# Kernel optimization log

Measured on AMD Instinct MI355X. Metric: run time of the kernel, lower is better.

Reference implementation:

```python
import jax, jax.numpy as jnp
import numpy as np

B, N, NODE_DIM, EDGE_DIM, H, L, Z, OUT = 4, 512, 16, 8, 64, 3, 64, 1
EPS = 1e-5  # torch BatchNorm1d default eps, training-mode batch stats


def _bn(x, g, b):
    # BatchNorm1d in training mode: biased batch mean/var over batch axis
    m = jnp.mean(x, axis=0)
    v = jnp.var(x, axis=0)
    return g * (x - m) * jax.lax.rsqrt(v + EPS) + b


def setup_inputs():
    keys = jax.random.split(jax.random.key(0), 16)

    def g(k, shape):
        fan = (shape[-2] + shape[-1]) if len(shape) >= 2 else 2 * shape[-1]
        return (jax.random.normal(k, shape) * np.sqrt(2.0 / fan)).astype(jnp.float32)

    return {
        'adj': (jax.random.uniform(keys[0], (B, N, N)) < 0.1).astype(jnp.float32),
        'node_feat': jax.random.normal(keys[1], (B, N, NODE_DIM), dtype=jnp.float32),
        'edge_feat': jax.random.normal(keys[2], (B, N, N, EDGE_DIM), dtype=jnp.float32),
        'nf1_w': g(keys[3], (NODE_DIM, 256)), 'nf1_b': jnp.zeros((256,), jnp.float32),
        'nf2_w': g(keys[4], (256, H)), 'nf2_b': jnp.zeros((H,), jnp.float32),
        'ef1_w': g(keys[5], (EDGE_DIM, 256)), 'ef1_b': jnp.zeros((256,), jnp.float32),
        'ef2_w': g(keys[6], (256, H)), 'ef2_b': jnp.zeros((H,), jnp.float32),
        'gcn_w': g(keys[7], (L, H, H)),
        'vn1_w': g(keys[8], (L, H, 2 * H)), 'vn1_b': jnp.zeros((L, 2 * H), jnp.float32),
        'vn1_g': jnp.ones((L, 2 * H), jnp.float32), 'vn1_be': jnp.zeros((L, 2 * H), jnp.float32),
        'vn2_w': g(keys[9], (L, 2 * H, H)), 'vn2_b': jnp.zeros((L, H), jnp.float32),
        'vn2_g': jnp.ones((L, H), jnp.float32), 'vn2_be': jnp.zeros((L, H), jnp.float32),
        'comb_w': g(keys[10], (L, 2 * H, H)), 'comb_b': jnp.zeros((L, H), jnp.float32),
        'lat1_w': g(keys[11], ((L + 1) * H, 256)), 'lat1_b': jnp.zeros((256,), jnp.float32),
        'lat2_w': g(keys[12], (256, Z)), 'lat2_b': jnp.zeros((Z,), jnp.float32),
        'fc1_w': g(keys[13], (Z, 512)), 'fc1_b': jnp.zeros((512,), jnp.float32),
        'fc2_w': g(keys[14], (512, OUT)), 'fc2_b': jnp.zeros((OUT,), jnp.float32),
    }


def _forward(adj, node_feat, edge_feat, nf1_w, nf1_b, nf2_w, nf2_b, ef1_w, ef1_b,
             ef2_w, ef2_b, gcn_w, vn1_w, vn1_b, vn1_g, vn1_be, vn2_w, vn2_b, vn2_g,
             vn2_be, comb_w, comb_b, lat1_w, lat1_b, lat2_w, lat2_b, fc1_w, fc1_b,
             fc2_w, fc2_b):
    # node / edge embedding MLPs
    nh = jnp.tanh(node_feat @ nf1_w + nf1_b)
    nh = jnp.tanh(nh @ nf2_w + nf2_b)                       # [B,N,H]
    eh = jnp.tanh(edge_feat @ ef1_w + ef1_b)
    eh = jnp.tanh(eh @ ef2_w + ef2_b)                       # [B,N,N,H]
    # einsum 'bijc,bjk->bik' sums over both j and c -> reduce c first
    e_sum = jnp.sum(eh, axis=-1)                            # [B,N,N]
    # GCN normalization: D = 1/rowsum(adj + I); identical every layer
    dinv = 1.0 / (jnp.sum(adj, axis=-1) + 1.0)
    adj_n = dinv[:, :, None] * adj                          # [B,N,N]
    hidden = nh
    alls = [nh]
    for l in range(L):
        hidden = jnp.tanh(adj_n @ (hidden @ gcn_w[l]))      # GraphConvSparse
        vn = jnp.mean(hidden, axis=1)                       # virtual-node pool [B,H]
        vn = jax.nn.relu(_bn(vn @ vn1_w[l] + vn1_b[l], vn1_g[l], vn1_be[l]))
        vn = jax.nn.relu(_bn(vn @ vn2_w[l] + vn2_b[l], vn2_g[l], vn2_be[l]))
        hidden = hidden + vn[:, None, :]                    # broadcast back to nodes
        gated = jnp.tanh(jnp.einsum('bij,bjk->bik', e_sum, hidden))
        hidden = jnp.tanh(jnp.concatenate([hidden, gated], axis=-1) @ comb_w[l] + comb_b[l])
        alls.append(hidden)
    lat = jnp.tanh(jnp.concatenate(alls, axis=-1) @ lat1_w + lat1_b)
    lat = jnp.tanh(lat @ lat2_w + lat2_b)                   # [B,N,Z]
    lat_sum = jnp.sum(lat, axis=1)                          # [B,Z]
    h = jnp.tanh(lat_sum @ fc1_w + fc1_b)
    predict = h @ fc2_w + fc2_b                             # [B,OUT]
    return predict, lat_sum


def reference(adj, node_feat, edge_feat, nf1_w, nf1_b, nf2_w, nf2_b, ef1_w, ef1_b,
              ef2_w, ef2_b, gcn_w, vn1_w, vn1_b, vn1_g, vn1_be, vn2_w, vn2_b, vn2_g,
              vn2_be, comb_w, comb_b, lat1_w, lat1_b, lat2_w, lat2_b, fc1_w, fc1_b,
              fc2_w, fc2_b):
    return _forward(adj, node_feat, edge_feat, nf1_w, nf1_b, nf2_w, nf2_b, ef1_w,
                    ef1_b, ef2_w, ef2_b, gcn_w, vn1_w, vn1_b, vn1_g, vn1_be, vn2_w,
                    vn2_b, vn2_g, vn2_be, comb_w, comb_b, lat1_w, lat1_b, lat2_w,
                    lat2_b, fc1_w, fc1_b, fc2_w, fc2_b)
```

## Files before the change

kernel.cpp:

```cpp
#include <hip/hip_runtime.h>
#include <math.h>

typedef unsigned short u16;
typedef unsigned int u32;

typedef __attribute__((ext_vector_type(8))) short short8;
typedef __attribute__((ext_vector_type(4))) float floatx4;

#define NTILES 16384

__device__ __forceinline__ float bfu(u16 u) { return __uint_as_float(((u32)u) << 16); }
__device__ __forceinline__ u16 f2bfs(float f) {
  u32 x = __float_as_uint(f);
  return (u16)((x + 0x7FFFu + ((x >> 16) & 1u)) >> 16);
}
__device__ __forceinline__ float tanh_fast(float x) {
  float e = __builtin_amdgcn_exp2f(x * 2.885390081777927f);
  return 1.0f - 2.0f * __builtin_amdgcn_rcpf(e + 1.0f);
}

__global__ __attribute__((amdgpu_flat_work_group_size(1024, 1024)))
__attribute__((amdgpu_waves_per_eu(4, 4)))
void k_edge(const float* __restrict__ ef,
    const float* __restrict__ w1, const float* __restrict__ b1,
    const float* __restrict__ w2, const float* __restrict__ b2,
    float* __restrict__ es32, u16* __restrict__ es16, int use16,
    int qt0, int qt1) {
  __shared__ __align__(16) short T1[16 * 2048];
  __shared__ __align__(16) short W2L[16384];
  __shared__ __align__(16) short W1L[2 * 2056];
  __shared__ __align__(16) float B1L[256];
  __shared__ __align__(16) float B2L[64];
  int t = threadIdx.x;
  int lane = t & 63, w = t >> 6, q = lane >> 4, r = lane & 15;

  for (int u = 0; u < 16; ++u) {
    int flat = u * 1024 + t;
    int k = flat >> 6, n = flat & 63;
    int c = k >> 3, j = k & 7;
    int physc = (c & 16) | ((c & 15) ^ (n & 15));
    W2L[(n * 32 + physc) * 8 + j] = (short)f2bfs(w2[flat]);
  }
  if (t < 512) {
    int hilo = t >> 8, idx = t & 255;
    int gu = idx >> 4, rr = idx & 15;
    int feat = (gu < 8) ? (rr * 8 + gu) : (120 + rr * 8 + gu);
    short8 v;
#pragma unroll
    for (int j = 0; j < 8; ++j) {
      float x = w1[j * 256 + feat];
      u32 xb = __float_as_uint(x);
      u16 hi = (u16)(xb >> 16);
      v[j] = hilo ? (short)f2bfs(x - bfu(hi)) : (short)hi;
    }
    *(short8*)&W1L[hilo * 2056 + idx * 8] = v;
  }
  if (t < 256) B1L[t] = b1[t];
  if (t < 64)  B2L[t] = b2[t];
  __syncthreads();

  short* t1w = &T1[w * 2048];
  const int hb = (q >> 1) * 2056;
  const int nw = gridDim.x * 16;
  int qt = qt0 + blockIdx.x * 16 + w;
  float4 e0, e1;
  {
    const float4* ep = (const float4*)(ef + (size_t)qt * 128 + (size_t)r * 8);
    e0 = ep[0]; e1 = ep[1];
  }

  for (; qt < qt1; qt += nw) {
    float ev[8] = {e0.x, e0.y, e0.z, e0.w, e1.x, e1.y, e1.z, e1.w};
    short8 af1;
#pragma unroll
    for (int j = 0; j < 8; ++j) {
      u32 xb = __float_as_uint(ev[j]);
      u16 hi = (u16)(xb >> 16);
      af1[j] = (q & 1) ? (short)f2bfs(ev[j] - bfu(hi)) : (short)hi;
    }
    int nqt = qt + nw;
    if (nqt < qt1) {
      const float4* ep = (const float4*)(ef + (size_t)nqt * 128 + (size_t)r * 8);
      e0 = ep[0]; e1 = ep[1];
    }
    floatx4 acc4[4];
#pragma unroll
    for (int nt = 0; nt < 4; ++nt) acc4[nt] = (floatx4){0.f, 0.f, 0.f, 0.f};
#pragma unroll
    for (int ph = 0; ph < 2; ++ph) {
      floatx4 c1[8];
#pragma unroll
      for (int u = 0; u < 8; ++u) c1[u] = (floatx4){0.f, 0.f, 0.f, 0.f};
#pragma unroll
      for (int u = 0; u < 8; ++u) {
        short8 bf = *(const short8*)&W1L[hb + ((ph * 8 + u) * 16 + r) * 8];
        c1[u] = __builtin_amdgcn_mfma_f32_16x16x32_bf16(af1, bf, c1[u], 0, 0, 0);
      }
      asm volatile("s_waitcnt lgkmcnt(0)" ::: "memory");
      __builtin_amdgcn_sched_barrier(0);
      const float4* bp = (const float4*)&B1L[ph * 128 + r * 8];
      float4 bA = bp[0], bB = bp[1];
      float bias[8] = {bA.x, bA.y, bA.z, bA.w, bB.x, bB.y, bB.z, bB.w};
#pragma unroll
      for (int reg = 0; reg < 4; ++reg) {
        u32 pk[4];
#pragma unroll
        for (int p2 = 0; p2 < 4; ++p2) {
          float va = tanh_fast(c1[2 * p2][reg] + bias[2 * p2]);
          float vb = tanh_fast(c1[2 * p2 + 1][reg] + bias[2 * p2 + 1]);
          u32 pr;
          asm("v_cvt_pk_bf16_f32 %0, %1, %2" : "=v"(pr) : "v"(va), "v"(vb));
          pk[p2] = pr;
        }
        int row = q * 4 + reg;
        int physc = r ^ row;
        int4 wa; wa.x = (int)pk[0]; wa.y = (int)pk[1]; wa.z = (int)pk[2]; wa.w = (int)pk[3];
        *(int4*)&t1w[(row * 16 + physc) * 8] = wa;
      }
      asm volatile("s_waitcnt lgkmcnt(0)" ::: "memory");
      __builtin_amdgcn_sched_barrier(0);
#pragma unroll
      for (int sm = 0; sm < 4; ++sm) {
        int cc = (4 * sm + q) ^ r;
        short8 af = *(const short8*)&t1w[(r * 16 + cc) * 8];
        int wc = ph * 16 + cc;
#pragma unroll
        for (int nt = 0; nt < 4; ++nt) {
          short8 bf = *(const short8*)&W2L[((nt * 16 + r) * 32 + wc) * 8];
          acc4[nt] = __builtin_amdgcn_mfma_f32_16x16x32_bf16(af, bf, acc4[nt], 0, 0, 0);
        }
      }
    }
    float s0 = 0.f, s1 = 0.f, s2 = 0.f, s3 = 0.f;
#pragma unroll
    for (int nt = 0; nt < 4; ++nt) {
      float bb = B2L[nt * 16 + r];
      s0 += tanh_fast(acc4[nt][0] + bb);
      s1 += tanh_fast(acc4[nt][1] + bb);
      s2 += tanh_fast(acc4[nt][2] + bb);
      s3 += tanh_fast(acc4[nt][3] + bb);
    }
#pragma unroll
    for (int off = 1; off < 16; off <<= 1) {
      s0 += __shfl_xor(s0, off, 64);
      s1 += __shfl_xor(s1, off, 64);
      s2 += __shfl_xor(s2, off, 64);
      s3 += __shfl_xor(s3, off, 64);
    }
    if (r == 0) {
      int base = qt * 16 + q * 4;
      if (use16) {
        es16[base] = f2bfs(s0); es16[base + 1] = f2bfs(s1);
        es16[base + 2] = f2bfs(s2); es16[base + 3] = f2bfs(s3);
      } else {
        float4 o; o.x = s0; o.y = s1; o.z = s2; o.w = s3;
        *(float4*)&es32[base] = o;
      }
    }
  }
}

__global__ __launch_bounds__(256) void k_pre(const float* __restrict__ nf,
    const float* __restrict__ w1, const float* __restrict__ b1,
    const float* __restrict__ w2, const float* __restrict__ b2,
    const float* __restrict__ gw, const float* __restrict__ adj,
    float* __restrict__ hid, u16* __restrict__ alls16, float* __restrict__ tmp,
    float* __restrict__ dinv, int* __restrict__ cnt) {
  __shared__ float nfx[4][16];
  __shared__ float t1[4][256];
  __shared__ float nh[4][64];
  int t = threadIdx.x;
  int node0 = blockIdx.x * 4;
  if (blockIdx.x == 0 && t < 16) cnt[t] = 0;
  if (t < 64) nfx[t >> 4][t & 15] = nf[node0 * 16 + t];
  __syncthreads();
  float b1t = b1[t];
  float a0 = b1t, a1 = b1t, a2 = b1t, a3 = b1t;
#pragma unroll
  for (int c = 0; c < 16; ++c) {
    float wv = w1[c * 256 + t];
    a0 += nfx[0][c] * wv; a1 += nfx[1][c] * wv;
    a2 += nfx[2][c] * wv; a3 += nfx[3][c] * wv;
  }
  t1[0][t] = tanh_fast(a0); t1[1][t] = tanh_fast(a1);
  t1[2][t] = tanh_fast(a2); t1[3][t] = tanh_fast(a3);
  __syncthreads();
  int nl = t >> 6, h = t & 63;
  {
    float acc = b2[h];
    for (int c = 0; c < 256; c += 4) {
      float4 xv = *(const float4*)&t1[nl][c];
      acc += xv.x * w2[c * 64 + h] + xv.y * w2[(c + 1) * 64 + h]
           + xv.z * w2[(c + 2) * 64 + h] + xv.w * w2[(c + 3) * 64 + h];
    }
    float v = tanh_fast(acc);
    int node = node0 + nl;
    hid[node * 64 + h] = v;
    alls16[node * 256 + h] = f2bfs(v);
    nh[nl][h] = v;
  }
  __syncthreads();
  {
    float g = 0.f;
    for (int c = 0; c < 64; ++c) g += nh[nl][c] * gw[c * 64 + h];
    tmp[(node0 + nl) * 64 + h] = g;
  }
  {
    int lane = t & 63, row = node0 + (t >> 6);
    float s = 0.f;
#pragma unroll
    for (int u = 0; u < 8; ++u) s += adj[(size_t)row * 512 + u * 64 + lane];
#pragma unroll
    for (int off = 32; off > 0; off >>= 1) s += __shfl_xor(s, off, 64);
    if (lane == 0) dinv[row] = 1.0f / (s + 1.0f);
  }
}

__global__ __launch_bounds__(256) void k_adjmm0(const float* __restrict__ adj,
    const float* __restrict__ X, const float* __restrict__ dinv,
    float* __restrict__ out, float* __restrict__ vnpart, int* cnt,
    const float* __restrict__ vw1, const float* __restrict__ vb1,
    const float* __restrict__ vg1, const float* __restrict__ vbe1,
    const float* __restrict__ vw2, const float* __restrict__ vb2,
    const float* __restrict__ vg2, const float* __restrict__ vbe2,
    float* __restrict__ vnout, int l) {
  __shared__ float Xt[64 * 64];
  __shared__ float Al[8 * 65];
  __shared__ floatx4 red4[256];
  __shared__ int isLast;
  int t = threadIdx.x;
  int b = blockIdx.x >> 6, it = blockIdx.x & 63;
  int hq = t & 15, slot = t >> 4, row = slot & 7, half = slot >> 3;
  floatx4 acc = (floatx4){0.f, 0.f, 0.f, 0.f};
  for (int jt = 0; jt < 8; ++jt) {
    __syncthreads();
    for (int u = 0; u < 16; ++u) {
      int idx = u * 256 + t;
      int jl = idx >> 6, hh = idx & 63;
      Xt[idx] = X[(b * 512 + jt * 64 + jl) * 64 + hh];
    }
#pragma unroll
    for (int u = 0; u < 2; ++u) {
      int idx = u * 256 + t;
      int il = idx >> 6, jl = idx & 63;
      Al[il * 65 + jl] = adj[((size_t)(b * 512 + it * 8 + il)) * 512 + jt * 64 + jl];
    }
    __syncthreads();
    const float* xp = &Xt[(half * 32) * 64 + hq * 4];
    const float* ap = &Al[row * 65 + half * 32];
#pragma unroll
    for (int jl = 0; jl < 32; ++jl) {
      floatx4 xv = *(const floatx4*)(xp + jl * 64);
      float a = ap[jl];
      acc[0] += a * xv[0]; acc[1] += a * xv[1];
      acc[2] += a * xv[2]; acc[3] += a * xv[3];
    }
  }
  red4[t] = acc;
  __syncthreads();
  if (t < 128) {
    floatx4 s = red4[t], s2 = red4[t + 128];
    int gr = b * 512 + it * 8 + row;
    float d = dinv[gr];
    floatx4 o;
#pragma unroll
    for (int i = 0; i < 4; ++i) o[i] = tanh_fast((s[i] + s2[i]) * d);
    *(floatx4*)&out[gr * 64 + hq * 4] = o;
    red4[t] = o;
  }
  __syncthreads();
  if (t < 16) {
    floatx4 ssum = (floatx4){0.f, 0.f, 0.f, 0.f};
#pragma unroll
    for (int r2 = 0; r2 < 8; ++r2) {
      floatx4 v = red4[r2 * 16 + t];
      ssum[0] += v[0]; ssum[1] += v[1]; ssum[2] += v[2]; ssum[3] += v[3];
    }
    *(floatx4*)&vnpart[(b * 64 + it) * 64 + t * 4] = ssum;
  }
  __threadfence();
  __syncthreads();
  if (t == 0) isLast = (atomicAdd(cnt, 1) == 255);
  __syncthreads();
  if (isLast) {
    __threadfence();
    float* x0 = Xt; float* x1 = Xt + 256; float* y1 = Xt + 768; float* x2 = Xt + 1280;
    {
      int bb = t >> 6, h = t & 63;
      float s = 0.f;
      for (int c = 0; c < 64; ++c) s += vnpart[(bb * 64 + c) * 64 + h];
      x0[t] = s * (1.0f / 512.0f);
    }
    __syncthreads();
    for (int rep = 0; rep < 2; ++rep) {
      int idx = rep * 256 + t;
      int bb = idx >> 7, j = idx & 127;
      float a = vb1[l * 128 + j];
      for (int h = 0; h < 64; ++h) a += x0[bb * 64 + h] * vw1[l * 8192 + h * 128 + j];
      x1[idx] = a;
    }
    __syncthreads();
    if (t < 128) {
      int j = t;
      float a = x1[j], bq = x1[128 + j], c = x1[256 + j], d = x1[384 + j];
      float m = 0.25f * (a + bq + c + d);
      float da = a - m, db = bq - m, dc = c - m, dd = d - m;
      float var = 0.25f * (da * da + db * db + dc * dc + dd * dd);
      float sc = vg1[l * 128 + j] / sqrtf(var + 1e-5f);
      float be = vbe1[l * 128 + j];
      y1[j]       = fmaxf(sc * da + be, 0.f);
      y1[128 + j] = fmaxf(sc * db + be, 0.f);
      y1[256 + j] = fmaxf(sc * dc + be, 0.f);
      y1[384 + j] = fmaxf(sc * dd + be, 0.f);
    }
    __syncthreads();
    {
      int bb = t >> 6, k = t & 63;
      float a = vb2[l * 64 + k];
      for (int j = 0; j < 128; ++j) a += y1[bb * 128 + j] * vw2[l * 8192 + j * 64 + k];
      x2[t] = a;
    }
    __syncthreads();
    if (t < 64) {
      int k = t;
      float a = x2[k], bq = x2[64 + k], c = x2[128 + k], d = x2[192 + k];
      float m = 0.25f * (a + bq + c + d);
      float da = a - m, db = bq - m, dc = c - m, dd = d - m;
      float var = 0.25f * (da * da + db * db + dc * dc + dd * dd);
      float sc = vg2[l * 64 + k] / sqrtf(var + 1e-5f);
      float be = vbe2[l * 64 + k];
      vnout[k]       = fmaxf(sc * da + be, 0.f);
      vnout[64 + k]  = fmaxf(sc * db + be, 0.f);
      vnout[128 + k] = fmaxf(sc * dc + be, 0.f);
      vnout[192 + k] = fmaxf(sc * dd + be, 0.f);
    }
  }
}

__global__ __launch_bounds__(256) void k_gate_comb(
    const float* __restrict__ es32, const u16* __restrict__ es16, int use16,
    const float* __restrict__ hid, const float* __restrict__ vnin,
    const float* __restrict__ cw, const float* __restrict__ cb,
    const float* __restrict__ gw_next,
    u16* __restrict__ alls16, float* __restrict__ tmpout, int l, int do_gcn) {
  __shared__ float Xt[64 * 64];
  __shared__ float Al[8 * 65];
  __shared__ floatx4 red4[256];
  __shared__ float gatedL[8 * 64];
  __shared__ float catL[8 * 128];
  __shared__ float hnL[8 * 64];
  int t = threadIdx.x;
  int b = blockIdx.x >> 6, it = blockIdx.x & 63;
  int hq = t & 15, slot = t >> 4, row = slot & 7, half = slot >> 3;
  floatx4 acc = (floatx4){0.f, 0.f, 0.f, 0.f};
  for (int jt = 0; jt < 8; ++jt) {
    __syncthreads();
    for (int u = 0; u < 16; ++u) {
      int idx = u * 256 + t;
      int jl = idx >> 6, hh = idx & 63;
      Xt[idx] = hid[(b * 512 + jt * 64 + jl) * 64 + hh] + vnin[b * 64 + hh];
    }
#pragma unroll
    for (int u = 0; u < 2; ++u) {
      int idx = u * 256 + t;
      int il = idx >> 6, jl = idx & 63;
      size_t ai = ((size_t)(b * 512 + it * 8 + il)) * 512 + jt * 64 + jl;
      Al[il * 65 + jl] = use16 ? bfu(es16[ai]) : es32[ai];
    }
    __syncthreads();
    const float* xp = &Xt[(half * 32) * 64 + hq * 4];
    const float* ap = &Al[row * 65 + half * 32];
#pragma unroll
    for (int jl = 0; jl < 32; ++jl) {
      floatx4 xv = *(const floatx4*)(xp + jl * 64);
      float a = ap[jl];
      acc[0] += a * xv[0]; acc[1] += a * xv[1];
      acc[2] += a * xv[2]; acc[3] += a * xv[3];
    }
  }
  red4[t] = acc;
  __syncthreads();
  if (t < 128) {
    floatx4 s = red4[t], s2 = red4[t + 128];
    floatx4 o;
#pragma unroll
    for (int i = 0; i < 4; ++i) o[i] = tanh_fast(s[i] + s2[i]);
    *(floatx4*)&gatedL[row * 64 + hq * 4] = o;
  }
  __syncthreads();
#pragma unroll
  for (int u = 0; u < 4; ++u) {
    int idx = u * 256 + t;
    int nl = idx >> 7, c = idx & 127;
    int node = b * 512 + it * 8 + nl;
    catL[idx] = (c < 64) ? (hid[node * 64 + c] + vnin[b * 64 + c])
                         : gatedL[nl * 64 + (c - 64)];
  }
  __syncthreads();
  int nl = t >> 6, h = t & 63;
  float a0 = cb[l * 64 + h], a1 = a0;
  const float* wp = cw + l * 8192 + h;
  for (int c = 0; c < 128; ++c) {
    float wv = wp[c * 64];
    a0 += catL[nl * 128 + c] * wv;
    a1 += catL[(nl + 4) * 128 + c] * wv;
  }
  float v0 = tanh_fast(a0), v1 = tanh_fast(a1);
  int n0 = b * 512 + it * 8 + nl, n1 = n0 + 4;
  alls16[n0 * 256 + (l + 1) * 64 + h] = f2bfs(v0);
  alls16[n1 * 256 + (l + 1) * 64 + h] = f2bfs(v1);
  if (do_gcn) {
    hnL[nl * 64 + h] = v0;
    hnL[(nl + 4) * 64 + h] = v1;
    __syncthreads();
    float g0 = 0.f, g1 = 0.f;
    for (int c = 0; c < 64; ++c) {
      float wv = gw_next[c * 64 + h];
      g0 += hnL[nl * 64 + c] * wv;
      g1 += hnL[(nl + 4) * 64 + c] * wv;
    }
    tmpout[n0 * 64 + h] = g0;
    tmpout[n1 * 64 + h] = g1;
  }
}

__global__ __launch_bounds__(512) void k_lat(const u16* __restrict__ alls16,
    const float* __restrict__ w1, const float* __restrict__ bb1,
    const float* __restrict__ w2, const float* __restrict__ bb2,
    float* __restrict__ latpart) {
  __shared__ float x[8][256];
  __shared__ float t1[8][256];
  __shared__ float red[8][256];
  int t = threadIdx.x;
  int g = t >> 8, tt = t & 255;
  int b = blockIdx.x >> 6, chunk = blockIdx.x & 63;
#pragma unroll
  for (int u = 0; u < 4; ++u)
    x[g * 4 + u][tt] = bfu(alls16[(size_t)(b * 512 + chunk * 8 + g * 4 + u) * 256 + tt]);
  __syncthreads();
  float a1[4];
  float bb = bb1[tt];
#pragma unroll
  for (int u = 0; u < 4; ++u) a1[u] = bb;
  for (int c = 0; c < 256; ++c) {
    float wv = w1[c * 256 + tt];
#pragma unroll
    for (int u = 0; u < 4; ++u) a1[u] += x[g * 4 + u][c] * wv;
  }
#pragma unroll
  for (int u = 0; u < 4; ++u) t1[g * 4 + u][tt] = tanh_fast(a1[u]);
  __syncthreads();
  int quar = tt >> 6, k = tt & 63, c0 = quar * 64;
  float a2[4];
#pragma unroll
  for (int u = 0; u < 4; ++u) a2[u] = 0.f;
  for (int c = 0; c < 64; ++c) {
    float wv = w2[(c0 + c) * 64 + k];
#pragma unroll
    for (int u = 0; u < 4; ++u) a2[u] += t1[g * 4 + u][c0 + c] * wv;
  }
#pragma unroll
  for (int u = 0; u < 4; ++u) red[g * 4 + u][tt] = a2[u];
  __syncthreads();
  if (t < 64) {
    float acc2 = 0.f;
    float b2v = bb2[t];
#pragma unroll
    for (int u = 0; u < 8; ++u) {
      float s = red[u][t] + red[u][t + 64] + red[u][t + 128] + red[u][t + 192] + b2v;
      acc2 += tanh_fast(s);
    }
    latpart[(b * 64 + chunk) * 64 + t] = acc2;
  }
}

__global__ __launch_bounds__(512) void k_final(const float* __restrict__ latpart,
    const float* __restrict__ f1w, const float* __restrict__ f1b,
    const float* __restrict__ f2w, const float* __restrict__ f2b,
    float* __restrict__ outp) {
  __shared__ float lred[512];
  __shared__ float ls[64];
  __shared__ float wred[8];
  int b = blockIdx.x, t = threadIdx.x;
  int z = t & 63, cg = t >> 6;
  float s = 0.f;
  for (int c = cg * 8; c < cg * 8 + 8; ++c) s += latpart[(b * 64 + c) * 64 + z];
  lred[t] = s;
  __syncthreads();
  if (t < 64) {
    float ssum = 0.f;
    for (int gg = 0; gg < 8; ++gg) ssum += lred[gg * 64 + t];
    ls[t] = ssum;
    outp[4 + b * 64 + t] = ssum;
  }
  __syncthreads();
  float acc = f1b[t];
  for (int zz = 0; zz < 64; ++zz) acc += ls[zz] * f1w[zz * 512 + t];
  float h = tanh_fast(acc);
  float p = h * f2w[t];
#pragma unroll
  for (int off = 32; off > 0; off >>= 1) p += __shfl_xor(p, off, 64);
  if ((t & 63) == 0) wred[t >> 6] = p;
  __syncthreads();
  if (t == 0) {
    float a = 0.f;
    for (int wv = 0; wv < 8; ++wv) a += wred[wv];
    outp[b] = a + f2b[0];
  }
}

extern "C" void kernel_launch(void* const* d_in, const int* in_sizes, int n_in,
                              void* d_out, int out_size, void* d_ws, size_t ws_size,
                              hipStream_t stream) {
  const float* adj       = (const float*)d_in[0];
  const float* node_feat = (const float*)d_in[1];
  const float* edge_feat = (const float*)d_in[2];
  const float* nf1_w = (const float*)d_in[3];
  const float* nf1_b = (const float*)d_in[4];
  const float* nf2_w = (const float*)d_in[5];
  const float* nf2_b = (const float*)d_in[6];
  const float* ef1_w = (const float*)d_in[7];
  const float* ef1_b = (const float*)d_in[8];
  const float* ef2_w = (const float*)d_in[9];
  const float* ef2_b = (const float*)d_in[10];
  const float* gcn_w = (const float*)d_in[11];
  const float* vn1_w = (const float*)d_in[12];
  const float* vn1_b = (const float*)d_in[13];
  const float* vn1_g = (const float*)d_in[14];
  const float* vn1_be = (const float*)d_in[15];
  const float* vn2_w = (const float*)d_in[16];
  const float* vn2_b = (const float*)d_in[17];
  const float* vn2_g = (const float*)d_in[18];
  const float* vn2_be = (const float*)d_in[19];
  const float* comb_w = (const float*)d_in[20];
  const float* comb_b = (const float*)d_in[21];
  const float* lat1_w = (const float*)d_in[22];
  const float* lat1_b = (const float*)d_in[23];
  const float* lat2_w = (const float*)d_in[24];
  const float* lat2_b = (const float*)d_in[25];
  const float* fc1_w = (const float*)d_in[26];
  const float* fc1_b = (const float*)d_in[27];
  const float* fc2_w = (const float*)d_in[28];
  const float* fc2_b = (const float*)d_in[29];

  const int use16 = (ws_size < (size_t)12 * 1024 * 1024) ? 1 : 0;
  char* p = (char*)d_ws;
  float* es32 = (float*)p;
  u16*   es16 = (u16*)p;
  size_t es_bytes = use16 ? (size_t)1048576 * 2 : (size_t)1048576 * 4;
  u16*   alls16  = (u16*)(p + es_bytes);
  float* hid     = (float*)(alls16 + 524288);
  float* tmp     = hid + 131072;
  float* dinv    = tmp + 131072;
  float* vnpart  = dinv + 2048;
  float* vn      = vnpart + 16384;
  float* latpart = vn + 256;
  int*   cnt     = (int*)(latpart + 16384);

  k_pre<<<512, 256, 0, stream>>>(node_feat, nf1_w, nf1_b, nf2_w, nf2_b,
                                 gcn_w, adj, hid, alls16, tmp, dinv, cnt);
  for (int d = 0; d < 8; ++d)
    k_edge<<<256, 1024, 0, stream>>>(edge_feat, ef1_w, ef1_b, ef2_w, ef2_b,
                                     es32, es16, use16,
                                     d * 8192, (d + 1) * 8192);
  for (int l = 0; l < 3; ++l) {
    k_adjmm0<<<256, 256, 0, stream>>>(adj, tmp, dinv, hid, vnpart, cnt + l,
        vn1_w, vn1_b, vn1_g, vn1_be, vn2_w, vn2_b, vn2_g, vn2_be, vn, l);
    k_gate_comb<<<256, 256, 0, stream>>>(es32, es16, use16, hid, vn,
        comb_w, comb_b, gcn_w + (l + 1) * 4096, alls16, tmp, l, (l < 2) ? 1 : 0);
  }
  k_lat<<<256, 512, 0, stream>>>(alls16, lat1_w, lat1_b, lat2_w, lat2_b, latpart);
  k_final<<<4, 512, 0, stream>>>(latpart, fc1_w, fc1_b, fc2_w, fc2_b,
                                 (float*)d_out);
}
```

Measured before the change: 468.5 us.

## Restructure adjacency matmuls to one wave per row with direct global loads

Rewrites the adj@X and edge-sum@hidden kernels so each 64-lane wave computes one output row, streaming the adjacency row as vector loads and reading X columns straight from global/L2 instead of staging tiles in shared memory. This doubles the grid to 512 blocks and drops most block-wide barriers. The virtual-node add is folded algebraically as rowsum(e)*vn, so it is no longer added per tile. The risk is more redundant global traffic for X, which no longer gets reuse from shared memory, and the wave-local LDS sync relies on s_waitcnt instead of __syncthreads.

```diff
diff --git a/kernel.cpp b/kernel.cpp
--- a/kernel.cpp
+++ b/kernel.cpp
@@ -224,71 +224,45 @@
     const float* __restrict__ vw2, const float* __restrict__ vb2,
     const float* __restrict__ vg2, const float* __restrict__ vbe2,
     float* __restrict__ vnout, int l) {
-  __shared__ float Xt[64 * 64];
-  __shared__ float Al[8 * 65];
-  __shared__ floatx4 red4[256];
+  __shared__ float vnp[4][64];
+  __shared__ float buf[1536];
   __shared__ int isLast;
   int t = threadIdx.x;
-  int b = blockIdx.x >> 6, it = blockIdx.x & 63;
-  int hq = t & 15, slot = t >> 4, row = slot & 7, half = slot >> 3;
-  floatx4 acc = (floatx4){0.f, 0.f, 0.f, 0.f};
-  for (int jt = 0; jt < 8; ++jt) {
-    __syncthreads();
-    for (int u = 0; u < 16; ++u) {
-      int idx = u * 256 + t;
-      int jl = idx >> 6, hh = idx & 63;
-      Xt[idx] = X[(b * 512 + jt * 64 + jl) * 64 + hh];
-    }
-#pragma unroll
-    for (int u = 0; u < 2; ++u) {
-      int idx = u * 256 + t;
-      int il = idx >> 6, jl = idx & 63;
-      Al[il * 65 + jl] = adj[((size_t)(b * 512 + it * 8 + il)) * 512 + jt * 64 + jl];
-    }
-    __syncthreads();
-    const float* xp = &Xt[(half * 32) * 64 + hq * 4];
-    const float* ap = &Al[row * 65 + half * 32];
-#pragma unroll
-    for (int jl = 0; jl < 32; ++jl) {
-      floatx4 xv = *(const floatx4*)(xp + jl * 64);
-      float a = ap[jl];
-      acc[0] += a * xv[0]; acc[1] += a * xv[1];
-      acc[2] += a * xv[2]; acc[3] += a * xv[3];
-    }
-  }
-  red4[t] = acc;
-  __syncthreads();
-  if (t < 128) {
-    floatx4 s = red4[t], s2 = red4[t + 128];
-    int gr = b * 512 + it * 8 + row;
-    float d = dinv[gr];
-    floatx4 o;
-#pragma unroll
-    for (int i = 0; i < 4; ++i) o[i] = tanh_fast((s[i] + s2[i]) * d);
-    *(floatx4*)&out[gr * 64 + hq * 4] = o;
-    red4[t] = o;
-  }
-  __syncthreads();
-  if (t < 16) {
-    floatx4 ssum = (floatx4){0.f, 0.f, 0.f, 0.f};
-#pragma unroll
-    for (int r2 = 0; r2 < 8; ++r2) {
-      floatx4 v = red4[r2 * 16 + t];
-      ssum[0] += v[0]; ssum[1] += v[1]; ssum[2] += v[2]; ssum[3] += v[3];
-    }
-    *(floatx4*)&vnpart[(b * 64 + it) * 64 + t * 4] = ssum;
+  int w = t >> 6, lane = t & 63;
+  int b = blockIdx.x >> 7, blk = blockIdx.x & 127;
+  int row = b * 512 + blk * 4 + w;
+  float d = dinv[row];
+  const float* ar = adj + (size_t)row * 512;
+  const float* xb = X + (size_t)b * 512 * 64;
+  float acc = 0.f;
+#pragma unroll 4
+  for (int j = 0; j < 512; j += 4) {
+    float4 a4 = *(const float4*)(ar + j);
+    float x0 = xb[(j + 0) * 64 + lane];
+    float x1 = xb[(j + 1) * 64 + lane];
+    float x2 = xb[(j + 2) * 64 + lane];
+    float x3 = xb[(j + 3) * 64 + lane];
+    acc += a4.x * x0 + a4.y * x1 + a4.z * x2 + a4.w * x3;
+  }
+  float o = tanh_fast(acc * d);
+  out[(size_t)row * 64 + lane] = o;
+  vnp[w][lane] = o;
+  __syncthreads();
+  if (t < 64) {
+    float s = vnp[0][t] + vnp[1][t] + vnp[2][t] + vnp[3][t];
+    vnpart[(b * 128 + blk) * 64 + t] = s;
   }
   __threadfence();
   __syncthreads();
-  if (t == 0) isLast = (atomicAdd(cnt, 1) == 255);
+  if (t == 0) isLast = (atomicAdd(cnt, 1) == 511);
   __syncthreads();
   if (isLast) {
     __threadfence();
-    float* x0 = Xt; float* x1 = Xt + 256; float* y1 = Xt + 768; float* x2 = Xt + 1280;
+    float* x0 = buf; float* x1 = buf + 256; float* y1 = buf + 768; float* x2 = buf + 1280;
     {
       int bb = t >> 6, h = t & 63;
       float s = 0.f;
-      for (int c = 0; c < 64; ++c) s += vnpart[(bb * 64 + c) * 64 + h];
+      for (int c = 0; c < 128; ++c) s += vnpart[(bb * 128 + c) * 64 + h];
       x0[t] = s * (1.0f / 512.0f);
     }
     __syncthreads();
@@ -302,9 +276,9 @@
     __syncthreads();
     if (t < 128) {
       int j = t;
-      float a = x1[j], bq = x1[128 + j], c = x1[256 + j], d = x1[384 + j];
-      float m = 0.25f * (a + bq + c + d);
-      float da = a - m, db = bq - m, dc = c - m, dd = d - m;
+      float a = x1[j], bq = x1[128 + j], c = x1[256 + j], d2 = x1[384 + j];
+      float m = 0.25f * (a + bq + c + d2);
+      float da = a - m, db = bq - m, dc = c - m, dd = d2 - m;
       float var = 0.25f * (da * da + db * db + dc * dc + dd * dd);
       float sc = vg1[l * 128 + j] / sqrtf(var + 1e-5f);
       float be = vbe1[l * 128 + j];
@@ -323,9 +297,9 @@
     __syncthreads();
     if (t < 64) {
       int k = t;
-      float a = x2[k], bq = x2[64 + k], c = x2[128 + k], d = x2[192 + k];
-      float m = 0.25f * (a + bq + c + d);
-      float da = a - m, db = bq - m, dc = c - m, dd = d - m;
+      float a = x2[k], bq = x2[64 + k], c = x2[128 + k], d2 = x2[192 + k];
+      float m = 0.25f * (a + bq + c + d2);
+      float da = a - m, db = bq - m, dc = c - m, dd = d2 - m;
       float var = 0.25f * (da * da + db * db + dc * dc + dd * dd);
       float sc = vg2[l * 64 + k] / sqrtf(var + 1e-5f);
       float be = vbe2[l * 64 + k];
@@ -343,84 +317,55 @@
     const float* __restrict__ cw, const float* __restrict__ cb,
     const float* __restrict__ gw_next,
     u16* __restrict__ alls16, float* __restrict__ tmpout, int l, int do_gcn) {
-  __shared__ float Xt[64 * 64];
-  __shared__ float Al[8 * 65];
-  __shared__ floatx4 red4[256];
-  __shared__ float gatedL[8 * 64];
-  __shared__ float catL[8 * 128];
-  __shared__ float hnL[8 * 64];
+  __shared__ float catL[4][128];
+  __shared__ float hnL[4][64];
   int t = threadIdx.x;
-  int b = blockIdx.x >> 6, it = blockIdx.x & 63;
-  int hq = t & 15, slot = t >> 4, row = slot & 7, half = slot >> 3;
-  floatx4 acc = (floatx4){0.f, 0.f, 0.f, 0.f};
-  for (int jt = 0; jt < 8; ++jt) {
-    __syncthreads();
-    for (int u = 0; u < 16; ++u) {
-      int idx = u * 256 + t;
-      int jl = idx >> 6, hh = idx & 63;
-      Xt[idx] = hid[(b * 512 + jt * 64 + jl) * 64 + hh] + vnin[b * 64 + hh];
-    }
-#pragma unroll
-    for (int u = 0; u < 2; ++u) {
-      int idx = u * 256 + t;
-      int il = idx >> 6, jl = idx & 63;
-      size_t ai = ((size_t)(b * 512 + it * 8 + il)) * 512 + jt * 64 + jl;
-      Al[il * 65 + jl] = use16 ? bfu(es16[ai]) : es32[ai];
-    }
-    __syncthreads();
-    const float* xp = &Xt[(half * 32) * 64 + hq * 4];
-    const float* ap = &Al[row * 65 + half * 32];
-#pragma unroll
-    for (int jl = 0; jl < 32; ++jl) {
-      floatx4 xv = *(const floatx4*)(xp + jl * 64);
-      float a = ap[jl];
-      acc[0] += a * xv[0]; acc[1] += a * xv[1];
-      acc[2] += a * xv[2]; acc[3] += a * xv[3];
-    }
-  }
-  red4[t] = acc;
-  __syncthreads();
-  if (t < 128) {
-    floatx4 s = red4[t], s2 = red4[t + 128];
-    floatx4 o;
-#pragma unroll
-    for (int i = 0; i < 4; ++i) o[i] = tanh_fast(s[i] + s2[i]);
-    *(floatx4*)&gatedL[row * 64 + hq * 4] = o;
-  }
-  __syncthreads();
-#pragma unroll
-  for (int u = 0; u < 4; ++u) {
-    int idx = u * 256 + t;
-    int nl = idx >> 7, c = idx & 127;
-    int node = b * 512 + it * 8 + nl;
-    catL[idx] = (c < 64) ? (hid[node * 64 + c] + vnin[b * 64 + c])
-                         : gatedL[nl * 64 + (c - 64)];
-  }
-  __syncthreads();
-  int nl = t >> 6, h = t & 63;
-  float a0 = cb[l * 64 + h], a1 = a0;
-  const float* wp = cw + l * 8192 + h;
-  for (int c = 0; c < 128; ++c) {
-    float wv = wp[c * 64];
-    a0 += catL[nl * 128 + c] * wv;
-    a1 += catL[(nl + 4) * 128 + c] * wv;
-  }
-  float v0 = tanh_fast(a0), v1 = tanh_fast(a1);
-  int n0 = b * 512 + it * 8 + nl, n1 = n0 + 4;
-  alls16[n0 * 256 + (l + 1) * 64 + h] = f2bfs(v0);
-  alls16[n1 * 256 + (l + 1) * 64 + h] = f2bfs(v1);
+  int w = t >> 6, lane = t & 63;
+  int b = blockIdx.x >> 7, blk = blockIdx.x & 127;
+  int row = b * 512 + blk * 4 + w;
+  float vnl = vnin[b * 64 + lane];
+  const float* hb = hid + (size_t)b * 512 * 64;
+  float acc = 0.f, asum = 0.f;
+  if (use16) {
+    const u16* er = es16 + (size_t)row * 512;
+#pragma unroll 4
+    for (int j = 0; j < 512; j += 4) {
+      uint2 u2 = *(const uint2*)(er + j);
+      float a0 = bfu((u16)(u2.x & 0xffffu)), a1 = bfu((u16)(u2.x >> 16));
+      float a2 = bfu((u16)(u2.y & 0xffffu)), a3 = bfu((u16)(u2.y >> 16));
+      acc += a0 * hb[(j + 0) * 64 + lane] + a1 * hb[(j + 1) * 64 + lane]
+           + a2 * hb[(j + 2) * 64 + lane] + a3 * hb[(j + 3) * 64 + lane];
+      asum += (a0 + a1) + (a2 + a3);
+    }
+  } else {
+    const float* er = es32 + (size_t)row * 512;
+#pragma unroll 4
+    for (int j = 0; j < 512; j += 4) {
+      float4 a4 = *(const float4*)(er + j);
+      acc += a4.x * hb[(j + 0) * 64 + lane] + a4.y * hb[(j + 1) * 64 + lane]
+           + a4.z * hb[(j + 2) * 64 + lane] + a4.w * hb[(j + 3) * 64 + lane];
+      asum += (a4.x + a4.y) + (a4.z + a4.w);
+    }
+  }
+  float gated = tanh_fast(acc + asum * vnl);
+  catL[w][lane] = hid[(size_t)row * 64 + lane] + vnl;
+  catL[w][64 + lane] = gated;
+  asm volatile("s_waitcnt lgkmcnt(0)" ::: "memory");
+  __builtin_amdgcn_sched_barrier(0);
+  float a = cb[l * 64 + lane];
+  const float* wp = cw + l * 8192 + lane;
+#pragma unroll 4
+  for (int c = 0; c < 128; ++c) a += catL[w][c] * wp[c * 64];
+  float v = tanh_fast(a);
+  alls16[(size_t)row * 256 + (l + 1) * 64 + lane] = f2bfs(v);
   if (do_gcn) {
-    hnL[nl * 64 + h] = v0;
-    hnL[(nl + 4) * 64 + h] = v1;
-    __syncthreads();
-    float g0 = 0.f, g1 = 0.f;
-    for (int c = 0; c < 64; ++c) {
-      float wv = gw_next[c * 64 + h];
-      g0 += hnL[nl * 64 + c] * wv;
-      g1 += hnL[(nl + 4) * 64 + c] * wv;
-    }
-    tmpout[n0 * 64 + h] = g0;
-    tmpout[n1 * 64 + h] = g1;
+    hnL[w][lane] = v;
+    asm volatile("s_waitcnt lgkmcnt(0)" ::: "memory");
+    __builtin_amdgcn_sched_barrier(0);
+    float g = 0.f;
+#pragma unroll 4
+    for (int c = 0; c < 64; ++c) g += hnL[w][c] * gw_next[c * 64 + lane];
+    tmpout[(size_t)row * 64 + lane] = g;
   }
 }
 
@@ -553,7 +498,7 @@
   float* tmp     = hid + 131072;
   float* dinv    = tmp + 131072;
   float* vnpart  = dinv + 2048;
-  float* vn      = vnpart + 16384;
+  float* vn      = vnpart + 32768;
   float* latpart = vn + 256;
   int*   cnt     = (int*)(latpart + 16384);
 
@@ -564,9 +509,9 @@
                                      es32, es16, use16,
                                      d * 8192, (d + 1) * 8192);
   for (int l = 0; l < 3; ++l) {
-    k_adjmm0<<<256, 256, 0, stream>>>(adj, tmp, dinv, hid, vnpart, cnt + l,
+    k_adjmm0<<<512, 256, 0, stream>>>(adj, tmp, dinv, hid, vnpart, cnt + l,
         vn1_w, vn1_b, vn1_g, vn1_be, vn2_w, vn2_b, vn2_g, vn2_be, vn, l);
-    k_gate_comb<<<256, 256, 0, stream>>>(es32, es16, use16, hid, vn,
+    k_gate_comb<<<512, 256, 0, stream>>>(es32, es16, use16, hid, vn,
         comb_w, comb_b, gcn_w + (l + 1) * 4096, alls16, tmp, l, (l < 2) ? 1 : 0);
   }
   k_lat<<<256, 512, 0, stream>>>(alls16, lat1_w, lat1_b, lat2_w, lat2_b, latpart);
```

Result: slower. 568.9 us (+21.4%).
